# Kernel tuning notes

Hardware: AMD Instinct MI355X
Metric: run time of the kernel (lower is better)

The kernel has to match this reference:

```python
import jax, jax.numpy as jnp
import numpy as np

NUM_GROUPS = 8   # num_groups1, recursive_index=False path
NUM_HEADS = 8


def setup_inputs() -> dict:
    key = jax.random.key(0)
    k1, k2, k3 = jax.random.split(key, 3)
    B, C, H, W = 4, 256, 64, 64
    x = jax.random.normal(k1, (B, C, H, W), dtype=jnp.float32)
    w_qkv = jax.random.normal(k2, (3 * C, C), dtype=jnp.float32) * 0.02
    w_proj = jax.random.normal(k3, (C, C), dtype=jnp.float32) * 0.02
    b_proj = jnp.zeros((C,), dtype=jnp.float32)
    return {"x": x, "w_qkv": w_qkv, "w_proj": w_proj, "b_proj": b_proj}


def reference(x, w_qkv, w_proj, b_proj):
    B, C, H, W = x.shape
    N = H * W
    G = NUM_GROUPS
    nh = NUM_HEADS
    hd = C // nh
    M = N // G
    scale = hd ** -0.5

    # b c h w -> b (h w) c
    xf = x.reshape(B, C, N).transpose(0, 2, 1)  # [B, N, C]

    # qkv linear (no bias), then split into groups / heads
    qkv = (xf @ w_qkv.T).reshape(B, G, M, 3, nh, hd)
    qkv = jnp.transpose(qkv, (3, 0, 1, 4, 2, 5))  # [3, B, G, nh, M, hd]
    q, k, v = qkv[0], qkv[1], qkv[2]

    # grouped multi-head attention, manual softmax
    attn = jax.nn.softmax(jnp.einsum('bghmd,bghnd->bghmn', q, k) * scale, axis=-1)
    out = jnp.einsum('bghmn,bghnd->bghmd', attn, v)

    # [B,G,nh,M,hd] -> [B,G,M,C] -> [B,N,C]
    out = out.transpose(0, 1, 3, 2, 4).reshape(B, N, C)

    out = out @ w_proj.T + b_proj

    # b (h w) c -> b c h w
    return out.transpose(0, 2, 1).reshape(B, C, H, W)
```

## Files before the change

kernel.cpp:

```cpp
#include <hip/hip_runtime.h>
#include <hip/hip_bf16.h>

#define Bb 4
#define Cc 256
#define Nn 4096
#define Gg 8
#define NHh 8
#define HDd 32
#define Mm 512

typedef __bf16 bf16_t;
typedef __bf16 bf16x2 __attribute__((ext_vector_type(2)));
typedef __bf16 bf16x4 __attribute__((ext_vector_type(4)));
typedef __bf16 bf16x8 __attribute__((ext_vector_type(8)));
typedef float f32x4 __attribute__((ext_vector_type(4)));

#define LSCALE (0.17677669529663687f * 1.44269504088896340f)

__device__ __forceinline__ void load_lds16(const bf16_t* g, bf16_t* l) {
  __builtin_amdgcn_global_load_lds(
      (const __attribute__((address_space(1))) void*)g,
      (__attribute__((address_space(3))) void*)l, 16, 0, 0);
}

__global__ __launch_bounds__(256) void prep_kernel(
    const float* __restrict__ x, bf16_t* __restrict__ xT,
    const float* __restrict__ wqkv, const float* __restrict__ wproj,
    bf16_t* __restrict__ wq_b, bf16_t* __restrict__ wp_b) {
  int bid = blockIdx.x, tid = threadIdx.x;
  if (bid >= 1024) {
    int i = (bid - 1024) * 256 + tid;
    wq_b[i] = (bf16_t)wqkv[i];
    if (i < Cc * Cc) wp_b[i] = (bf16_t)wproj[i];
    return;
  }
  __shared__ float t[64][65];
  int b = bid >> 8, c0 = ((bid >> 6) & 3) * 64, n0 = (bid & 63) * 64;
  const float* xp = x + ((long long)b * Cc + c0) * Nn + n0;
#pragma unroll
  for (int it = 0; it < 4; ++it) {
    int idx = it * 256 + tid;
    int r = idx >> 4, col = (idx & 15) * 4;
    f32x4 v = *(const f32x4*)&xp[(long long)r * Nn + col];
    t[r][col] = v[0];
    t[r][col + 1] = v[1];
    t[r][col + 2] = v[2];
    t[r][col + 3] = v[3];
  }
  __syncthreads();
  bf16_t* op = xT + ((long long)b * Nn + n0) * Cc + c0;
#pragma unroll
  for (int it = 0; it < 2; ++it) {
    int idx = it * 256 + tid;
    int n = idx >> 3, cg = (idx & 7) * 8;
    bf16x8 w;
#pragma unroll
    for (int j = 0; j < 8; ++j) w[j] = (bf16_t)t[cg + j][n];
    *(bf16x8*)&op[(long long)n * Cc + cg] = w;
  }
}

__global__ __launch_bounds__(256, 4) void qkv_gemm_kernel(
    const bf16_t* __restrict__ xT, const bf16_t* __restrict__ wqb,
    bf16_t* __restrict__ Qh, bf16_t* __restrict__ Kh, bf16_t* __restrict__ Vh) {
  __shared__ bf16_t As[2][64 * 32];
  __shared__ bf16_t Bs[2][256 * 32];
  int bid = blockIdx.x;
  int m0 = (bid / 3) * 64;
  int n0 = (bid % 3) * 256;
  int tid = threadIdx.x, lane = tid & 63, wid = tid >> 6;
  int quad = lane >> 4, l16 = lane & 15;
  int wn = wid * 64;

  f32x4 acc[4][4];
#pragma unroll
  for (int i = 0; i < 4; ++i)
#pragma unroll
    for (int j = 0; j < 4; ++j) acc[i][j] = (f32x4){0.f, 0.f, 0.f, 0.f};

  int scol = (lane & 3) * 8;
  int arow = lane >> 2;
  auto stage = [&](int bufi, int k0) {
    load_lds16(&xT[(long long)(m0 + wid * 16 + arow) * Cc + k0 + scol],
               &As[bufi][wid * 512]);
#pragma unroll
    for (int r = 0; r < 4; ++r) {
      int ch = wid * 4 + r;
      load_lds16(&wqb[(long long)(n0 + ch * 16 + arow) * Cc + k0 + scol],
                 &Bs[bufi][ch * 512]);
    }
  };

  stage(0, 0);
  __syncthreads();
  for (int t = 0; t < 8; ++t) {
    if (t < 7) stage((t + 1) & 1, (t + 1) * 32);
    const bf16_t* Ap = As[t & 1];
    const bf16_t* Bp = Bs[t & 1];
    bf16x8 a[4], b[4];
#pragma unroll
    for (int i = 0; i < 4; ++i)
      a[i] = *(const bf16x8*)&Ap[(i * 16 + l16) * 32 + quad * 8];
#pragma unroll
    for (int j = 0; j < 4; ++j)
      b[j] = *(const bf16x8*)&Bp[(wn + j * 16 + l16) * 32 + quad * 8];
#pragma unroll
    for (int i = 0; i < 4; ++i)
#pragma unroll
      for (int j = 0; j < 4; ++j)
        acc[i][j] = __builtin_amdgcn_mfma_f32_16x16x32_bf16(a[i], b[j], acc[i][j], 0, 0, 0);
    __syncthreads();
  }

  if (n0 < 512) {
    const bool isQ = (n0 == 0);
#pragma unroll
    for (int i = 0; i < 4; ++i) {
#pragma unroll
      for (int j = 0; j < 4; ++j) {
        int f = wn + j * 16 + l16;
        int hh = f >> 5, d = f & 31;
#pragma unroll
        for (int r = 0; r < 4; ++r) {
          int row = m0 + i * 16 + quad * 4 + r;
          int bb = row >> 12, gg = (row >> 9) & 7, m = row & 511;
          long long hb = (long long)((bb << 6) | (gg << 3) | hh) * (Mm * HDd);
          float v = acc[i][j][r];
          if (isQ)
            Qh[hb + m * HDd + d] = (bf16_t)(v * LSCALE);
          else
            Kh[hb + m * HDd + d] = (bf16_t)v;
        }
      }
    }
  } else {
#pragma unroll
    for (int i = 0; i < 4; ++i) {
#pragma unroll
      for (int j = 0; j < 4; ++j) {
        int f = wn + j * 16 + l16;
        int hh = f >> 5, d = f & 31;
        int row = m0 + i * 16 + quad * 4;
        int bb = row >> 12, gg = (row >> 9) & 7, m = row & 511;
        long long hb = (long long)((bb << 6) | (gg << 3) | hh) * (Mm * HDd);
        bf16x4 w;
#pragma unroll
        for (int r = 0; r < 4; ++r) w[r] = (bf16_t)acc[i][j][r];
        *(bf16x4*)&Vh[hb + (long long)d * Mm + m] = w;
      }
    }
  }
}

__global__ __launch_bounds__(256, 4) void attn_kernel(
    const bf16_t* __restrict__ Qh, const bf16_t* __restrict__ Kh,
    const bf16_t* __restrict__ Vh, bf16_t* __restrict__ Oa) {
  __shared__ bf16_t Ks[256 * 32];
  __shared__ bf16_t Vs[32 * 264];
  int gid = blockIdx.x;
  int ms = gid & 3, head = gid >> 2;
  int h = head & 7, g = (head >> 3) & 7, b = head >> 6;
  int tid = threadIdx.x, lane = tid & 63, wid = tid >> 6;
  int quad = lane >> 4, l16 = lane & 15;

  const bf16_t* Kg = Kh + (long long)head * (Mm * HDd);
  const bf16_t* Vg = Vh + (long long)head * (Mm * HDd);
  const bf16_t* Qg = Qh + (long long)head * (Mm * HDd) + (ms * 128 + wid * 32) * HDd;

  bf16x8 qa = *(const bf16x8*)&Qg[l16 * HDd + quad * 8];
  bf16x8 qb = *(const bf16x8*)&Qg[(16 + l16) * HDd + quad * 8];

  bf16x8 ones;
#pragma unroll
  for (int i = 0; i < 8; ++i) ones[i] = (bf16_t)1.0f;

  int rp0 = ((l16 >> 2) << 3) | (l16 & 3);
  const bf16_t* Kp0 = &Ks[rp0 * HDd + quad * 8];
  const bf16_t* Kp1 = Kp0 + 4 * HDd;
  const bf16_t* VsL = &Vs[l16 * 264 + quad * 8];
  const bf16_t* VsH = &Vs[(16 + l16) * 264 + quad * 8];
  const f32x4 zero = (f32x4){0.f, 0.f, 0.f, 0.f};

  f32x4 oLa = zero, oHa = zero, oLb = zero, oHb = zero;
  f32x4 ra = zero, rb = zero;

#pragma unroll 1
  for (int ph = 0; ph < 2; ++ph) {
    __syncthreads();
#pragma unroll
    for (int it = 0; it < 4; ++it) {
      int ch = wid * 4 + it;
      load_lds16(&Kg[ph * 8192 + ch * 512 + lane * 8], &Ks[ch * 512]);
    }
#pragma unroll
    for (int i = 0; i < 4; ++i) {
      int idx = i * 256 + tid;
      int d = idx >> 5, c16 = idx & 31;
      bf16x8 v = *(const bf16x8*)&Vg[d * Mm + ph * 256 + c16 * 8];
      *(bf16x8*)&Vs[d * 264 + c16 * 8] = v;
    }
    __syncthreads();

#pragma unroll
    for (int c = 0; c < 8; ++c) {
      int nb = c * 32;
      bf16x8 kf0 = *(const bf16x8*)&Kp0[nb * HDd];
      bf16x8 kf1 = *(const bf16x8*)&Kp1[nb * HDd];
      f32x4 sa0 = __builtin_amdgcn_mfma_f32_16x16x32_bf16(kf0, qa, zero, 0, 0, 0);
      f32x4 sa1 = __builtin_amdgcn_mfma_f32_16x16x32_bf16(kf1, qa, zero, 0, 0, 0);
      f32x4 sb0 = __builtin_amdgcn_mfma_f32_16x16x32_bf16(kf0, qb, zero, 0, 0, 0);
      f32x4 sb1 = __builtin_amdgcn_mfma_f32_16x16x32_bf16(kf1, qb, zero, 0, 0, 0);
      bf16x8 pa, pb;
#pragma unroll
      for (int r = 0; r < 4; ++r) {
        pa[r] = (bf16_t)__builtin_exp2f(sa0[r]);
        pa[4 + r] = (bf16_t)__builtin_exp2f(sa1[r]);
        pb[r] = (bf16_t)__builtin_exp2f(sb0[r]);
        pb[4 + r] = (bf16_t)__builtin_exp2f(sb1[r]);
      }
      bf16x8 vL = *(const bf16x8*)&VsL[nb];
      bf16x8 vH = *(const bf16x8*)&VsH[nb];
      oLa = __builtin_amdgcn_mfma_f32_16x16x32_bf16(vL, pa, oLa, 0, 0, 0);
      oHa = __builtin_amdgcn_mfma_f32_16x16x32_bf16(vH, pa, oHa, 0, 0, 0);
      oLb = __builtin_amdgcn_mfma_f32_16x16x32_bf16(vL, pb, oLb, 0, 0, 0);
      oHb = __builtin_amdgcn_mfma_f32_16x16x32_bf16(vH, pb, oHb, 0, 0, 0);
      ra = __builtin_amdgcn_mfma_f32_16x16x32_bf16(ones, pa, ra, 0, 0, 0);
      rb = __builtin_amdgcn_mfma_f32_16x16x32_bf16(ones, pb, rb, 0, 0, 0);
    }
  }

  float inva = 1.f / ra[0], invb = 1.f / rb[0];

  long long orowa =
      ((long long)(b * Nn + g * Mm + ms * 128 + wid * 32 + l16)) * Cc + h * HDd;
  long long orowb = orowa + 16 * Cc;
  bf16x4 wLa, wHa, wLb, wHb;
#pragma unroll
  for (int r = 0; r < 4; ++r) {
    wLa[r] = (bf16_t)(oLa[r] * inva);
    wHa[r] = (bf16_t)(oHa[r] * inva);
    wLb[r] = (bf16_t)(oLb[r] * invb);
    wHb[r] = (bf16_t)(oHb[r] * invb);
  }
  *(bf16x4*)&Oa[orowa + quad * 4] = wLa;
  *(bf16x4*)&Oa[orowa + 16 + quad * 4] = wHa;
  *(bf16x4*)&Oa[orowb + quad * 4] = wLb;
  *(bf16x4*)&Oa[orowb + 16 + quad * 4] = wHb;
}

__global__ __launch_bounds__(256, 4) void proj_kernel(
    const bf16_t* __restrict__ Wp, const bf16_t* __restrict__ Oa,
    float* __restrict__ out, const float* __restrict__ bias) {
  __shared__ bf16_t As[2][256 * 32];
  __shared__ bf16_t Bs[2][64 * 32];
  int tid = threadIdx.x, lane = tid & 63, wid = tid >> 6;
  int quad = lane >> 4, l16 = lane & 15;
  int z = blockIdx.z;
  const bf16_t* Bt = Oa + (long long)z * Nn * Cc;
  int n0 = blockIdx.x * 64;
  int wm = wid * 64;

  f32x4 acc[4][4];
#pragma unroll
  for (int i = 0; i < 4; ++i)
#pragma unroll
    for (int j = 0; j < 4; ++j) acc[i][j] = (f32x4){0.f, 0.f, 0.f, 0.f};

  int scol = (lane & 3) * 8;
  int arow = lane >> 2;
  auto stage = [&](int bufi, int k0) {
#pragma unroll
    for (int r = 0; r < 4; ++r) {
      int ch = wid * 4 + r;
      load_lds16(&Wp[(long long)(ch * 16 + arow) * Cc + k0 + scol],
                 &As[bufi][ch * 512]);
    }
    load_lds16(&Bt[(long long)(n0 + wid * 16 + arow) * Cc + k0 + scol],
               &Bs[bufi][wid * 512]);
  };

  stage(0, 0);
  __syncthreads();
  for (int t = 0; t < 8; ++t) {
    if (t < 7) stage((t + 1) & 1, (t + 1) * 32);
    const bf16_t* Ap = As[t & 1];
    const bf16_t* Bp = Bs[t & 1];
    bf16x8 a[4], b[4];
#pragma unroll
    for (int i = 0; i < 4; ++i)
      a[i] = *(const bf16x8*)&Ap[(wm + i * 16 + l16) * 32 + quad * 8];
#pragma unroll
    for (int j = 0; j < 4; ++j)
      b[j] = *(const bf16x8*)&Bp[(j * 16 + l16) * 32 + quad * 8];
#pragma unroll
    for (int i = 0; i < 4; ++i)
#pragma unroll
      for (int j = 0; j < 4; ++j)
        acc[i][j] = __builtin_amdgcn_mfma_f32_16x16x32_bf16(a[i], b[j], acc[i][j], 0, 0, 0);
    __syncthreads();
  }

#pragma unroll
  for (int i = 0; i < 4; ++i) {
#pragma unroll
    for (int j = 0; j < 4; ++j) {
      int col = n0 + j * 16 + l16;
#pragma unroll
      for (int r = 0; r < 4; ++r) {
        int row = wm + i * 16 + quad * 4 + r;
        out[(long long)z * (Cc * Nn) + (long long)row * Nn + col] =
            acc[i][j][r] + bias[row];
      }
    }
  }
}

extern "C" void kernel_launch(void* const* d_in, const int* in_sizes, int n_in,
                              void* d_out, int out_size, void* d_ws, size_t ws_size,
                              hipStream_t stream) {
  (void)in_sizes; (void)n_in; (void)out_size; (void)ws_size;
  const float* x = (const float*)d_in[0];
  const float* w_qkv = (const float*)d_in[1];
  const float* w_proj = (const float*)d_in[2];
  const float* b_proj = (const float*)d_in[3];
  float* out = (float*)d_out;

  char* ws = (char*)d_ws;
  bf16_t* xT  = (bf16_t*)(ws);
  bf16_t* wqb = (bf16_t*)(ws + 8388608);
  bf16_t* wpb = (bf16_t*)(ws + 8781824);
  bf16_t* Qh  = (bf16_t*)(ws + 8912896);
  bf16_t* Kh  = (bf16_t*)(ws + 17301504);
  bf16_t* Vh  = (bf16_t*)(ws + 25690112);
  bf16_t* Oa  = (bf16_t*)(ws + 34078720);

  prep_kernel<<<1792, 256, 0, stream>>>(x, xT, w_qkv, w_proj, wqb, wpb);
  qkv_gemm_kernel<<<768, 256, 0, stream>>>(xT, wqb, Qh, Kh, Vh);
  attn_kernel<<<1024, 256, 0, stream>>>(Qh, Kh, Vh, Oa);
  proj_kernel<<<dim3(64, 1, 4), 256, 0, stream>>>(wpb, Oa, out, b_proj);
}
```

Before: 124.5 us.

## Stage Q/K epilogue through LDS and split proj GEMM into smaller tiles

The QKV GEMM epilogue for Q and K now writes accumulators into a padded LDS tile, then stores them back out as 16-byte vector writes per head row. Before, each thread did scattered 2-byte global stores. The projection kernel changes from 256x64 tiles over 256 blocks to 64x64 tiles over 1024 blocks. Each wave now computes a 64x16 slice, which gives more parallelism and less LDS per block, at the cost of lower arithmetic intensity per block and more redundant loads of Oa.

```diff
diff --git a/kernel.cpp b/kernel.cpp
--- a/kernel.cpp
+++ b/kernel.cpp
@@ -63,8 +63,7 @@
 __global__ __launch_bounds__(256, 4) void qkv_gemm_kernel(
     const bf16_t* __restrict__ xT, const bf16_t* __restrict__ wqb,
     bf16_t* __restrict__ Qh, bf16_t* __restrict__ Kh, bf16_t* __restrict__ Vh) {
-  __shared__ bf16_t As[2][64 * 32];
-  __shared__ bf16_t Bs[2][256 * 32];
+  __shared__ bf16_t smem[20480];
   int bid = blockIdx.x;
   int m0 = (bid / 3) * 64;
   int n0 = (bid % 3) * 256;
@@ -82,12 +81,12 @@
   int arow = lane >> 2;
   auto stage = [&](int bufi, int k0) {
     load_lds16(&xT[(long long)(m0 + wid * 16 + arow) * Cc + k0 + scol],
-               &As[bufi][wid * 512]);
+               &smem[bufi * 2048 + wid * 512]);
 #pragma unroll
     for (int r = 0; r < 4; ++r) {
       int ch = wid * 4 + r;
       load_lds16(&wqb[(long long)(n0 + ch * 16 + arow) * Cc + k0 + scol],
-                 &Bs[bufi][ch * 512]);
+                 &smem[4096 + bufi * 8192 + ch * 512]);
     }
   };
 
@@ -95,8 +94,8 @@
   __syncthreads();
   for (int t = 0; t < 8; ++t) {
     if (t < 7) stage((t + 1) & 1, (t + 1) * 32);
-    const bf16_t* Ap = As[t & 1];
-    const bf16_t* Bp = Bs[t & 1];
+    const bf16_t* Ap = &smem[(t & 1) * 2048];
+    const bf16_t* Bp = &smem[4096 + (t & 1) * 8192];
     bf16x8 a[4], b[4];
 #pragma unroll
     for (int i = 0; i < 4; ++i)
@@ -114,24 +113,28 @@
 
   if (n0 < 512) {
     const bool isQ = (n0 == 0);
-#pragma unroll
-    for (int i = 0; i < 4; ++i) {
+    const float s = isQ ? LSCALE : 1.0f;
+#pragma unroll
+    for (int i = 0; i < 4; ++i)
 #pragma unroll
       for (int j = 0; j < 4; ++j) {
         int f = wn + j * 16 + l16;
-        int hh = f >> 5, d = f & 31;
 #pragma unroll
         for (int r = 0; r < 4; ++r) {
-          int row = m0 + i * 16 + quad * 4 + r;
-          int bb = row >> 12, gg = (row >> 9) & 7, m = row & 511;
-          long long hb = (long long)((bb << 6) | (gg << 3) | hh) * (Mm * HDd);
-          float v = acc[i][j][r];
-          if (isQ)
-            Qh[hb + m * HDd + d] = (bf16_t)(v * LSCALE);
-          else
-            Kh[hb + m * HDd + d] = (bf16_t)v;
+          int lm = i * 16 + quad * 4 + r;
+          smem[lm * 264 + f] = (bf16_t)(acc[i][j][r] * s);
         }
       }
+    __syncthreads();
+    int lm = tid >> 2, d0 = (tid & 3) * 8;
+    int row = m0 + lm;
+    int bb = row >> 12, gg = (row >> 9) & 7, m = row & 511;
+    bf16_t* dst = isQ ? Qh : Kh;
+#pragma unroll
+    for (int hh = 0; hh < 8; ++hh) {
+      long long hb = (long long)((bb << 6) | (gg << 3) | hh) * (Mm * HDd);
+      bf16x8 w = *(bf16x8*)&smem[lm * 264 + hh * 32 + d0];
+      *(bf16x8*)&dst[hb + m * HDd + d0] = w;
     }
   } else {
 #pragma unroll
@@ -251,30 +254,23 @@
 __global__ __launch_bounds__(256, 4) void proj_kernel(
     const bf16_t* __restrict__ Wp, const bf16_t* __restrict__ Oa,
     float* __restrict__ out, const float* __restrict__ bias) {
-  __shared__ bf16_t As[2][256 * 32];
+  __shared__ bf16_t As[2][64 * 32];
   __shared__ bf16_t Bs[2][64 * 32];
   int tid = threadIdx.x, lane = tid & 63, wid = tid >> 6;
   int quad = lane >> 4, l16 = lane & 15;
   int z = blockIdx.z;
   const bf16_t* Bt = Oa + (long long)z * Nn * Cc;
-  int n0 = blockIdx.x * 64;
-  int wm = wid * 64;
-
-  f32x4 acc[4][4];
-#pragma unroll
-  for (int i = 0; i < 4; ++i)
-#pragma unroll
-    for (int j = 0; j < 4; ++j) acc[i][j] = (f32x4){0.f, 0.f, 0.f, 0.f};
+  int m0 = blockIdx.y * 64, n0 = blockIdx.x * 64;
+
+  f32x4 acc[4];
+#pragma unroll
+  for (int i = 0; i < 4; ++i) acc[i] = (f32x4){0.f, 0.f, 0.f, 0.f};
 
   int scol = (lane & 3) * 8;
   int arow = lane >> 2;
   auto stage = [&](int bufi, int k0) {
-#pragma unroll
-    for (int r = 0; r < 4; ++r) {
-      int ch = wid * 4 + r;
-      load_lds16(&Wp[(long long)(ch * 16 + arow) * Cc + k0 + scol],
-                 &As[bufi][ch * 512]);
-    }
+    load_lds16(&Wp[(long long)(m0 + wid * 16 + arow) * Cc + k0 + scol],
+               &As[bufi][wid * 512]);
     load_lds16(&Bt[(long long)(n0 + wid * 16 + arow) * Cc + k0 + scol],
                &Bs[bufi][wid * 512]);
   };
@@ -285,32 +281,25 @@
     if (t < 7) stage((t + 1) & 1, (t + 1) * 32);
     const bf16_t* Ap = As[t & 1];
     const bf16_t* Bp = Bs[t & 1];
-    bf16x8 a[4], b[4];
-#pragma unroll
-    for (int i = 0; i < 4; ++i)
-      a[i] = *(const bf16x8*)&Ap[(wm + i * 16 + l16) * 32 + quad * 8];
-#pragma unroll
-    for (int j = 0; j < 4; ++j)
-      b[j] = *(const bf16x8*)&Bp[(j * 16 + l16) * 32 + quad * 8];
-#pragma unroll
-    for (int i = 0; i < 4; ++i)
-#pragma unroll
-      for (int j = 0; j < 4; ++j)
-        acc[i][j] = __builtin_amdgcn_mfma_f32_16x16x32_bf16(a[i], b[j], acc[i][j], 0, 0, 0);
+    bf16x8 a[4], b;
+#pragma unroll
+    for (int i = 0; i < 4; ++i)
+      a[i] = *(const bf16x8*)&Ap[(i * 16 + l16) * 32 + quad * 8];
+    b = *(const bf16x8*)&Bp[(wid * 16 + l16) * 32 + quad * 8];
+#pragma unroll
+    for (int i = 0; i < 4; ++i)
+      acc[i] = __builtin_amdgcn_mfma_f32_16x16x32_bf16(a[i], b, acc[i], 0, 0, 0);
     __syncthreads();
   }
 
 #pragma unroll
   for (int i = 0; i < 4; ++i) {
-#pragma unroll
-    for (int j = 0; j < 4; ++j) {
-      int col = n0 + j * 16 + l16;
-#pragma unroll
-      for (int r = 0; r < 4; ++r) {
-        int row = wm + i * 16 + quad * 4 + r;
-        out[(long long)z * (Cc * Nn) + (long long)row * Nn + col] =
-            acc[i][j][r] + bias[row];
-      }
+    int col = n0 + wid * 16 + l16;
+#pragma unroll
+    for (int r = 0; r < 4; ++r) {
+      int row = m0 + i * 16 + quad * 4 + r;
+      out[(long long)z * (Cc * Nn) + (long long)row * Nn + col] =
+          acc[i][r] + bias[row];
     }
   }
 }
@@ -337,5 +326,5 @@
   prep_kernel<<<1792, 256, 0, stream>>>(x, xT, w_qkv, w_proj, wqb, wpb);
   qkv_gemm_kernel<<<768, 256, 0, stream>>>(xT, wqb, Qh, Kh, Vh);
   attn_kernel<<<1024, 256, 0, stream>>>(Qh, Kh, Vh, Oa);
-  proj_kernel<<<dim3(64, 1, 4), 256, 0, stream>>>(wpb, Oa, out, b_proj);
-}
+  proj_kernel<<<dim3(64, 4, 4), 256, 0, stream>>>(wpb, Oa, out, b_proj);
+}
```

Result: no change. 122.4 us (-1.7%).
